# Kernel tuning notes

Measured on AMD Instinct MI355X. Metric: run time of the kernel, lower is better.

The kernel has to match this reference:

```python
import jax, jax.numpy as jnp
import numpy as np

B, DIM, H, W = 16, 96, 64, 64
HID = 2 * DIM          # ffn_expansion_factor = 2
BN_EPS = 1e-5
LN_EPS = 1e-6


def _gelu(x):
    return jax.nn.gelu(x, approximate=False)  # torch F.gelu default = exact erf


def _ln(x, g, b):
    m = jnp.mean(x, axis=-1, keepdims=True)
    v = jnp.mean((x - m) ** 2, axis=-1, keepdims=True)
    return (x - m) / jnp.sqrt(v + LN_EPS) * g + b


def _dwconv2d(x, w, b):
    # x: (B,C,H,W), w: (C,1,kh,kw) depthwise
    C = x.shape[1]
    kh, kw = w.shape[2], w.shape[3]
    y = jax.lax.conv_general_dilated(
        x, w, (1, 1), [(kh // 2, kh // 2), (kw // 2, kw // 2)],
        dimension_numbers=('NCHW', 'OIHW', 'NCHW'), feature_group_count=C)
    return y + b[None, :, None, None]


def _conv_along_c(z, w, b):
    # z: (N,1,C); w: (8,1,k) -> conv over spectral/channel axis (Conv3d with (1,1,k) kernel)
    k = w.shape[2]
    y = jax.lax.conv_general_dilated(z, w, (1,), [(k // 2, k // 2)],
                                     dimension_numbers=('NCH', 'OIH', 'NCH'))
    return y + b[None, :, None]


def _bn_branch(y, g, bb):
    # eval-mode BatchNorm3d with running_mean=0, running_var=1; y: (N,8,C)
    return _gelu(y * (g / jnp.sqrt(1.0 + BN_EPS))[None, :, None] + bb[None, :, None])


def _patch_embed(z, w3a, b3a, bn3a_g, bn3a_b, w3b, b3b, bn3b_g, bn3b_b,
                 w3c, b3c, bn3c_g, bn3c_b, w2, b2, bn2_g, bn2_b):
    # z: (b,h,w,c) NHWC; PatchEmbedLayerSpa
    b_, h_, w_, c_ = z.shape
    zf = z.reshape(-1, 1, c_)
    f1 = _bn_branch(_conv_along_c(zf, w3a, b3a), bn3a_g, bn3a_b)
    f2 = _bn_branch(_conv_along_c(zf, w3b, b3b), bn3b_g, bn3b_b)
    f3 = _bn_branch(_conv_along_c(zf, w3c, b3c), bn3c_g, bn3c_b)
    cat = jnp.concatenate([f1, f2, f3], axis=1).reshape(b_, h_, w_, 24, c_)
    # 1x1 Conv2d over flattened (c y) -> dim; einsum replaces rearrange + conv
    y = jnp.einsum('bhwoy,doy->bhwd', cat, w2) + b2
    y = _gelu(y * (bn2_g / jnp.sqrt(1.0 + BN_EPS)) + bn2_b)  # eval BatchNorm2d + GELU
    return y + z


def _ffn(t, pin_w, pin_b, dw_w, dw_b, pout_w, pout_b):
    # Restormer GDFN; t: (b, c, X, Y) NCHW
    u = jnp.einsum('bcxy,oc->boxy', t, pin_w) + pin_b[None, :, None, None]
    u = _dwconv2d(u, dw_w, dw_b)
    u1, u2 = jnp.split(u, 2, axis=1)
    g = _gelu(u1) * u2
    return jnp.einsum('bcxy,oc->boxy', g, pout_w) + pout_b[None, :, None, None]


def setup_inputs() -> dict:
    key = jax.random.key(0)
    ks = iter(jax.random.split(key, 48))
    nrm = lambda shape, s=0.02: jax.random.normal(next(ks), shape, jnp.float32) * s
    d = {}
    d['x'] = jax.random.normal(next(ks), (B, DIM, H, W), jnp.float32)
    d['pos_w'] = nrm((DIM, 1, 3, 3)); d['pos_b'] = jnp.zeros((DIM,), jnp.float32)
    for n in ('ln1', 'ln2', 'ln3'):
        d[n + '_g'] = jnp.ones((DIM,), jnp.float32)
        d[n + '_b'] = jnp.zeros((DIM,), jnp.float32)
    for n, k in (('a', 3), ('b', 5), ('c', 7)):
        d['w3' + n] = nrm((8, 1, k)); d['b3' + n] = jnp.zeros((8,), jnp.float32)
        d['bn3' + n + '_g'] = jnp.ones((8,), jnp.float32)
        d['bn3' + n + '_b'] = jnp.zeros((8,), jnp.float32)
    d['w2'] = nrm((DIM, 24, DIM)); d['b2'] = jnp.zeros((DIM,), jnp.float32)
    d['bn2_g'] = jnp.ones((DIM,), jnp.float32); d['bn2_b'] = jnp.zeros((DIM,), jnp.float32)
    d['pin_w'] = nrm((2 * HID, DIM)); d['pin_b'] = jnp.zeros((2 * HID,), jnp.float32)
    d['dw_w'] = nrm((2 * HID, 1, 3, 3)); d['dw_b'] = jnp.zeros((2 * HID,), jnp.float32)
    d['pout_w'] = nrm((DIM, HID)); d['pout_b'] = jnp.zeros((DIM,), jnp.float32)
    return d


def reference(x, pos_w, pos_b, ln1_g, ln1_b, ln2_g, ln2_b, ln3_g, ln3_b,
              w3a, b3a, bn3a_g, bn3a_b, w3b, b3b, bn3b_g, bn3b_b,
              w3c, b3c, bn3c_g, bn3c_b, w2, b2, bn2_g, bn2_b,
              pin_w, pin_b, dw_w, dw_b, pout_w, pout_b):
    # pos embed dwconv + residual (NCHW)
    x = x + _dwconv2d(x, pos_w, pos_b)
    y = jnp.transpose(x, (0, 2, 3, 1))  # NHWC
    # attn4(norm3(y)) returns its input (bug in source: `out = rearrange(x, ...)`)
    y = y + _ln(y, ln3_g, ln3_b)
    # attn(norm1(y)) returns PatchEmbedLayerSpa(norm1(y)) (same bug in MGEFE)
    y = y + _patch_embed(_ln(y, ln1_g, ln1_b), w3a, b3a, bn3a_g, bn3a_b,
                         w3b, b3b, bn3b_g, bn3b_b, w3c, b3c, bn3c_g, bn3c_b,
                         w2, b2, bn2_g, bn2_b)
    y = _ln(y, ln2_g, ln2_b)
    t = jnp.transpose(y, (0, 3, 2, 1))  # (b,c,w,h) per source permute(0,3,2,1)
    f = _ffn(t, pin_w, pin_b, dw_w, dw_b, pout_w, pout_b)
    f = jnp.transpose(f, (0, 2, 3, 1))  # (b,w,h,c)
    y = f + f
    return jnp.transpose(y, (0, 3, 1, 2))  # (b,c,w,h)
```

## Files before the change

kernel.cpp:

```cpp
#include <hip/hip_runtime.h>


using bf16x8 = __attribute__((ext_vector_type(8))) short;
using f32x4  = __attribute__((ext_vector_type(4))) float;
using f32x2  = __attribute__((ext_vector_type(2))) float;

struct P {
  const float *x, *pos_w, *pos_b;
  const float *ln1g, *ln1b, *ln2g, *ln2b, *ln3g, *ln3b;
  const float *w3a, *b3a, *bn3ag, *bn3ab;
  const float *w3b, *b3b, *bn3bg, *bn3bb;
  const float *w3c, *b3c, *bn3cg, *bn3cb;
  const float *w2, *b2, *bn2g, *bn2b;
  const float *pin_w, *pin_b, *dw_w, *dw_b, *pout_w, *pout_b;
  unsigned short *u;
  unsigned short *w2f;
  unsigned short *pinf;
  unsigned short *poutf;
  float *dwt;
  float *out;
};

__device__ __forceinline__ unsigned short f2bf(float f) {
  unsigned int v = __float_as_uint(f);
  v += 0x7fffu + ((v >> 16) & 1u);
  return (unsigned short)(v >> 16);
}
__device__ __forceinline__ float bf2f(unsigned short s) {
  return __uint_as_float(((unsigned int)s) << 16);
}
__device__ __forceinline__ unsigned int cvtpk(f32x2 g) {
  unsigned int pk;
  asm("v_cvt_pk_bf16_f32 %0, %1, %2" : "=v"(pk) : "v"(g.x), "v"(g.y));
  return pk;
}

__device__ __forceinline__ f32x2 gelu2p(f32x2 x) {
  f32x2 u = x * 0.70710678118654752f;
  f32x2 s = __builtin_elementwise_min(u * u, f32x2{1.f, 1.f});
  f32x2 pq = __builtin_elementwise_fma(s, f32x2{1.1283585149e-1f, 1.1283585149e-1f},
                                       f32x2{-3.7612625824e-1f, -3.7612625824e-1f});
  pq = __builtin_elementwise_fma(pq, s, f32x2{1.1283791657f, 1.1283791657f});
  f32x2 xh = x * 0.5f;
  return __builtin_elementwise_fma(xh, u * pq, xh);
}

__device__ __forceinline__ void swz_decode(int bid, int& b, int& s) {
  int xcd = bid & 7, idx = bid >> 3;
  b = xcd * 2 + (idx >> 6);
  s = idx & 63;
}

__global__ __launch_bounds__(256) void prep(P p) {
  int id = blockIdx.x * 256 + threadIdx.x;
  if (id < 221184) {
    int j = id & 7, l = (id >> 3) & 63, r = id >> 9;
    int ks = r % 3; r /= 3; int nt = r % 6, o = r / 6;
    int d = nt * 16 + (l & 15), y = ks * 32 + (l >> 4) * 8 + j;
    p.w2f[id] = f2bf(p.w2[(d * 24 + o) * 96 + y]);
  } else if (id < 258048) {
    int id2 = id - 221184;
    int j = id2 & 7, l = (id2 >> 3) & 63, r = id2 >> 9;
    int ks = r % 3, nt = r / 3;
    int o = nt * 16 + (l & 15), k = ks * 32 + (l >> 4) * 8 + j;
    p.pinf[id2] = f2bf(p.pin_w[o * 96 + k]);
  } else if (id < 276480) {
    int id3 = id - 258048;
    int j = id3 & 7, l = (id3 >> 3) & 63, r = id3 >> 9;
    int ks = r % 6, mt = r / 6;
    int d = mt * 16 + (l & 15), cc = ks * 32 + (l >> 4) * 8 + j;
    p.poutf[id3] = f2bf(p.pout_w[d * 192 + cc]);
  } else if (id < 279936) {
    int id4 = id - 276480;
    int tap = id4 / 384, c = id4 - tap * 384;
    p.dwt[id4] = p.dw_w[c * 9 + tap];
  }
}

template <int KSZ>
__device__ __forceinline__ void k2_cat(const float* __restrict__ w3, float b3v,
    float bng, float bnb, float rs, unsigned short* buf,
    const float (&zw)[30], int px, int c0) {
  float sc = bng * rs;
  float wr[KSZ];
  #pragma unroll
  for (int k = 0; k < KSZ; ++k) wr[k] = w3[k] * sc;
  float bias0 = fmaf(b3v, sc, bnb);
  constexpr int OFF = 3 - KSZ / 2;
  unsigned int packed[12];
  #pragma unroll
  for (int e2 = 0; e2 < 12; ++e2) {
    f32x2 f = {bias0, bias0};
    #pragma unroll
    for (int k = 0; k < KSZ; ++k) {
      f32x2 zp = {zw[2 * e2 + OFF + k], zw[2 * e2 + 1 + OFF + k]};
      f = __builtin_elementwise_fma(f32x2{wr[k], wr[k]}, zp, f);
    }
    packed[e2] = cvtpk(gelu2p(f));
  }
  uint4* cw = (uint4*)(buf + px * 104 + c0);
  cw[0] = *(uint4*)&packed[0];
  cw[1] = *(uint4*)&packed[4];
  cw[2] = *(uint4*)&packed[8];
}

template <int KSZ_NEXT, bool LAST>
__device__ __forceinline__ void k2_step(
    const P& p, int o, const float* __restrict__ w3n, float b3n,
    float bngn, float bnbn, float rs,
    const unsigned short* cur, unsigned short* nxt, const float (&zw)[30],
    int px, int c0, int nt0, int ar0, int ar1, f32x4 (&acc)[2][3]) {
  int lane = (threadIdx.x & 63);
  const unsigned short* wf = p.w2f + (size_t)o * 9216 + lane * 8;
  bf16x8 Ba[3], Bb[3];
  #pragma unroll
  for (int n = 0; n < 3; ++n)
    Ba[n] = *(const bf16x8*)(wf + ((nt0 + n) * 3 + 0) * 512);

  if (!LAST)
    k2_cat<KSZ_NEXT>(w3n, b3n, bngn, bnbn, rs, nxt, zw, px, c0);

  #pragma unroll
  for (int n = 0; n < 3; ++n)
    Bb[n] = *(const bf16x8*)(wf + ((nt0 + n) * 3 + 1) * 512);
  {
    bf16x8 a0 = *(const bf16x8*)&cur[ar0];
    bf16x8 a1 = *(const bf16x8*)&cur[ar1];
    #pragma unroll
    for (int n = 0; n < 3; ++n) {
      acc[0][n] = __builtin_amdgcn_mfma_f32_16x16x32_bf16(a0, Ba[n], acc[0][n], 0, 0, 0);
      acc[1][n] = __builtin_amdgcn_mfma_f32_16x16x32_bf16(a1, Ba[n], acc[1][n], 0, 0, 0);
    }
  }
  #pragma unroll
  for (int n = 0; n < 3; ++n)
    Ba[n] = *(const bf16x8*)(wf + ((nt0 + n) * 3 + 2) * 512);
  {
    bf16x8 a0 = *(const bf16x8*)&cur[ar0 + 32];
    bf16x8 a1 = *(const bf16x8*)&cur[ar1 + 32];
    #pragma unroll
    for (int n = 0; n < 3; ++n) {
      acc[0][n] = __builtin_amdgcn_mfma_f32_16x16x32_bf16(a0, Bb[n], acc[0][n], 0, 0, 0);
      acc[1][n] = __builtin_amdgcn_mfma_f32_16x16x32_bf16(a1, Bb[n], acc[1][n], 0, 0, 0);
    }
  }
  {
    bf16x8 a0 = *(const bf16x8*)&cur[ar0 + 64];
    bf16x8 a1 = *(const bf16x8*)&cur[ar1 + 64];
    #pragma unroll
    for (int n = 0; n < 3; ++n) {
      acc[0][n] = __builtin_amdgcn_mfma_f32_16x16x32_bf16(a0, Ba[n], acc[0][n], 0, 0, 0);
      acc[1][n] = __builtin_amdgcn_mfma_f32_16x16x32_bf16(a1, Ba[n], acc[1][n], 0, 0, 0);
    }
  }
  __syncthreads();
}

__global__ __launch_bounds__(256) void k2(P p) {
  __shared__ __align__(16) char smraw[26624];
  unsigned short* cat0 = (unsigned short*)smraw;
  unsigned short* cat1 = (unsigned short*)(smraw + 13312);
  float*          t1   = (float*)smraw;

  int b, h; swz_decode(blockIdx.x, b, h);
  int t = threadIdx.x, lane = t & 63, wv = t >> 6;
  int px = t >> 2, sub = t & 3, c0 = sub * 24;
  const float* xb = p.x + (size_t)b * 96 * 4096;

  if (t < 192) {
    int c = t >> 1, w0 = (t & 1) * 32;
    const float* xc = xb + (size_t)c * 4096;
    float win[3][34];
    #pragma unroll
    for (int r = 0; r < 3; ++r) {
      int hh = h - 1 + r;
      bool v = (hh >= 0 && hh < 64);
      const float* row = xc + hh * 64;
      #pragma unroll
      for (int i = 0; i < 8; ++i) {
        float4 q = v ? *(const float4*)(row + w0 + i * 4) : make_float4(0,0,0,0);
        win[r][1+i*4] = q.x; win[r][2+i*4] = q.y;
        win[r][3+i*4] = q.z; win[r][4+i*4] = q.w;
      }
      win[r][0]  = (v && w0 > 0)  ? row[w0 - 1]  : 0.f;
      win[r][33] = (v && w0 < 32) ? row[w0 + 32] : 0.f;
    }
    float wt[9];
    #pragma unroll
    for (int i = 0; i < 9; ++i) wt[i] = p.pos_w[c * 9 + i];
    float pb = p.pos_b[c];
    #pragma unroll
    for (int w = 0; w < 32; ++w) {
      float acc = pb;
      #pragma unroll
      for (int r = 0; r < 3; ++r)
        #pragma unroll
        for (int j = 0; j < 3; ++j)
          acc = fmaf(wt[r * 3 + j], win[r][w + j], acc);
      t1[c * 65 + w0 + w] = win[1][w + 1] + acc;
    }
  }
  __syncthreads();

  float vv[24];
  float zw[30];
  {
    float s1 = 0.f, s2 = 0.f;
    #pragma unroll
    for (int i = 0; i < 24; ++i) {
      float q = t1[(c0 + i) * 65 + px];
      vv[i] = q; s1 += q; s2 += q * q;
    }
    s1 += __shfl_xor(s1, 1); s1 += __shfl_xor(s1, 2);
    s2 += __shfl_xor(s2, 1); s2 += __shfl_xor(s2, 2);
    float m = s1 * (1.f / 96.f);
    float r = rsqrtf(fmaf(-m, m, s2 * (1.f / 96.f)) + 1e-6f);
    float t1s = 0.f, t2s = 0.f;
    #pragma unroll
    for (int i = 0; i < 24; ++i) {
      int c = c0 + i;
      float y = vv[i] + fmaf((vv[i] - m) * r, p.ln3g[c], p.ln3b[c]);
      vv[i] = y; t1s += y; t2s += y * y;
    }
    t1s += __shfl_xor(t1s, 1); t1s += __shfl_xor(t1s, 2);
    t2s += __shfl_xor(t2s, 1); t2s += __shfl_xor(t2s, 2);
    float m1 = t1s * (1.f / 96.f);
    float r1 = rsqrtf(fmaf(-m1, m1, t2s * (1.f / 96.f)) + 1e-6f);
    #pragma unroll
    for (int i = 0; i < 24; ++i) {
      int c = c0 + i;
      zw[3 + i] = fmaf((vv[i] - m1) * r1, p.ln1g[c], p.ln1b[c]);
    }
  }
  {
    float a0 = __shfl(zw[24], lane - 1), a1 = __shfl(zw[25], lane - 1),
          a2 = __shfl(zw[26], lane - 1);
    float b0 = __shfl(zw[3], lane + 1), b1 = __shfl(zw[4], lane + 1),
          b2 = __shfl(zw[5], lane + 1);
    bool lo = (sub > 0), hi = (sub < 3);
    zw[0] = lo ? a0 : 0.f; zw[1] = lo ? a1 : 0.f; zw[2] = lo ? a2 : 0.f;
    zw[27] = hi ? b0 : 0.f; zw[28] = hi ? b1 : 0.f; zw[29] = hi ? b2 : 0.f;
  }
  __syncthreads();

  const float rs = rsqrtf(1.f + 1e-5f);
  const int m0 = (wv >> 1) * 32, nt0 = (wv & 1) * 3;
  const int lm = lane & 15, lq = lane >> 4;
  const int ar0 = (m0 + lm) * 104 + lq * 8, ar1 = ar0 + 16 * 104;
  f32x4 acc[2][3];
  #pragma unroll
  for (int m = 0; m < 2; ++m)
    #pragma unroll
    for (int n = 0; n < 3; ++n) acc[m][n] = (f32x4){0.f, 0.f, 0.f, 0.f};

  k2_cat<3>(p.w3a, p.b3a[0], p.bn3ag[0], p.bn3ab[0], rs, cat0, zw, px, c0);
  __syncthreads();

  for (int o = 0; o < 7; ++o)
    k2_step<3, false>(p, o, p.w3a + (o + 1) * 3, p.b3a[o + 1],
                      p.bn3ag[o + 1], p.bn3ab[o + 1], rs,
                      (o & 1) ? cat1 : cat0, (o & 1) ? cat0 : cat1,
                      zw, px, c0, nt0, ar0, ar1, acc);
  k2_step<5, false>(p, 7, p.w3b, p.b3b[0], p.bn3bg[0], p.bn3bb[0], rs,
                    cat1, cat0, zw, px, c0, nt0, ar0, ar1, acc);
  for (int o = 8; o < 15; ++o)
    k2_step<5, false>(p, o, p.w3b + (o - 7) * 5, p.b3b[o - 7],
                      p.bn3bg[o - 7], p.bn3bb[o - 7], rs,
                      (o & 1) ? cat1 : cat0, (o & 1) ? cat0 : cat1,
                      zw, px, c0, nt0, ar0, ar1, acc);
  k2_step<7, false>(p, 15, p.w3c, p.b3c[0], p.bn3cg[0], p.bn3cb[0], rs,
                    cat1, cat0, zw, px, c0, nt0, ar0, ar1, acc);
  for (int o = 16; o < 23; ++o)
    k2_step<7, false>(p, o, p.w3c + (o - 15) * 7, p.b3c[o - 15],
                      p.bn3cg[o - 15], p.bn3cb[o - 15], rs,
                      (o & 1) ? cat1 : cat0, (o & 1) ? cat0 : cat1,
                      zw, px, c0, nt0, ar0, ar1, acc);
  k2_step<3, true>(p, 23, p.w3a, 0.f, 0.f, 0.f, rs,
                   cat1, cat0, zw, px, c0, nt0, ar0, ar1, acc);

  #pragma unroll
  for (int mi = 0; mi < 2; ++mi)
    #pragma unroll
    for (int n = 0; n < 3; ++n) {
      int d = (nt0 + n) * 16 + lm;
      float sc2 = p.bn2g[d] * rs, sh2 = p.bn2b[d], bias = p.b2[d];
      int pxb = m0 + mi * 16 + lq * 4;
      unsigned int pk01 = cvtpk(gelu2p(f32x2{fmaf(acc[mi][n][0] + bias, sc2, sh2),
                                             fmaf(acc[mi][n][1] + bias, sc2, sh2)}));
      unsigned int pk23 = cvtpk(gelu2p(f32x2{fmaf(acc[mi][n][2] + bias, sc2, sh2),
                                             fmaf(acc[mi][n][3] + bias, sc2, sh2)}));
      cat0[(pxb+0) * 104 + d] = (unsigned short)(pk01 & 0xffffu);
      cat0[(pxb+1) * 104 + d] = (unsigned short)(pk01 >> 16);
      cat0[(pxb+2) * 104 + d] = (unsigned short)(pk23 & 0xffffu);
      cat0[(pxb+3) * 104 + d] = (unsigned short)(pk23 >> 16);
    }
  __syncthreads();

  {
    const unsigned int* gsrc = (const unsigned int*)(cat0 + px * 104 + c0);
    float s1 = 0.f, s2 = 0.f;
    #pragma unroll
    for (int i2 = 0; i2 < 6; ++i2) {
      unsigned int w0 = gsrc[i2 * 2], w1 = gsrc[i2 * 2 + 1];
      float g0 = __uint_as_float(w0 << 16), g1 = __uint_as_float(w0 & 0xffff0000u);
      float g2 = __uint_as_float(w1 << 16), g3 = __uint_as_float(w1 & 0xffff0000u);
      float y0v = g0 + zw[3 + i2*4 + 0] + vv[i2*4 + 0];
      float y1v = g1 + zw[3 + i2*4 + 1] + vv[i2*4 + 1];
      float y2v = g2 + zw[3 + i2*4 + 2] + vv[i2*4 + 2];
      float y3v = g3 + zw[3 + i2*4 + 3] + vv[i2*4 + 3];
      vv[i2*4+0] = y0v; vv[i2*4+1] = y1v; vv[i2*4+2] = y2v; vv[i2*4+3] = y3v;
      s1 += y0v + y1v + y2v + y3v;
      s2 += y0v*y0v + y1v*y1v + y2v*y2v + y3v*y3v;
    }
    s1 += __shfl_xor(s1, 1); s1 += __shfl_xor(s1, 2);
    s2 += __shfl_xor(s2, 1); s2 += __shfl_xor(s2, 2);
    float m = s1 * (1.f / 96.f);
    float r = rsqrtf(fmaf(-m, m, s2 * (1.f / 96.f)) + 1e-6f);
    unsigned int* dst = (unsigned int*)(cat1 + px * 104 + c0);
    #pragma unroll
    for (int i = 0; i < 12; ++i) {
      int c = c0 + 2 * i;
      f32x2 y3p = {fmaf((vv[2*i]   - m) * r, p.ln2g[c],     p.ln2b[c]),
                   fmaf((vv[2*i+1] - m) * r, p.ln2g[c + 1], p.ln2b[c + 1])};
      dst[i] = cvtpk(y3p);
    }
  }
  __syncthreads();

  {
    const int mt = wv;
    bf16x8 B3[3];
    #pragma unroll
    for (int ks = 0; ks < 3; ++ks)
      B3[ks] = *(const bf16x8*)&cat1[(mt * 16 + lm) * 104 + ks * 32 + lq * 8];
    unsigned short* ubh = p.u + (size_t)b * 1572864 + h * 384;
    const int w = mt * 16 + lm;
    unsigned short* urow = ubh + (size_t)w * 24576 + lq * 4;

    bf16x8 An[3];
    const unsigned short* pf0 = p.pinf + lane * 8;
    #pragma unroll
    for (int ks = 0; ks < 3; ++ks)
      An[ks] = *(const bf16x8*)(pf0 + ks * 512);
    for (int nt = 0; nt < 24; ++nt) {
      bf16x8 Af[3] = {An[0], An[1], An[2]};
      if (nt < 23) {
        const unsigned short* pf = p.pinf + ((nt + 1) * 3) * 512 + lane * 8;
        #pragma unroll
        for (int ks = 0; ks < 3; ++ks)
          An[ks] = *(const bf16x8*)(pf + ks * 512);
      }
      f32x4 a4 = (f32x4){0.f, 0.f, 0.f, 0.f};
      #pragma unroll
      for (int ks = 0; ks < 3; ++ks)
        a4 = __builtin_amdgcn_mfma_f32_16x16x32_bf16(Af[ks], B3[ks], a4, 0, 0, 0);
      float4 pbq = *(const float4*)(p.pin_b + nt * 16 + lq * 4);
      unsigned int lo = cvtpk(f32x2{a4[0] + pbq.x, a4[1] + pbq.y});
      unsigned int hi = cvtpk(f32x2{a4[2] + pbq.z, a4[3] + pbq.w});
      *(uint2*)(urow + nt * 16) = make_uint2(lo, hi);
    }
  }
}

__global__ __launch_bounds__(192) void k4(P p) {
  __shared__ __align__(16) char sm4[40960];
  float*          dwl = (float*)sm4;
  float*          dbl = (float*)(sm4 + 13824);
  unsigned short* gl  = (unsigned short*)(sm4 + 15360);

  int b, w; swz_decode(blockIdx.x, b, w);
  int t = threadIdx.x, lane = t & 63, wv = t >> 6;
  const unsigned short* ub = p.u + (size_t)b * 1572864;

  for (int id = t; id < 3456; id += 192) dwl[id] = p.dwt[id];
  for (int id = t; id < 384; id += 192) dbl[id] = p.dw_b[id];
  __syncthreads();

  {
    int g = t / 24, cb = t - g * 24;
    int c0 = cb * 8, hb = g * 8;
    float4 b1a = *(const float4*)&dbl[c0],       b1b = *(const float4*)&dbl[c0 + 4];
    float4 b2a = *(const float4*)&dbl[192 + c0], b2b = *(const float4*)&dbl[196 + c0];
    const bf16x8 zv = {0,0,0,0,0,0,0,0};
    for (int kk = 0; kk < 4; ++kk) {
      int h0 = hb + kk * 2;
      float v1[2][8], v2[2][8];
      #pragma unroll
      for (int hr = 0; hr < 2; ++hr) {
        v1[hr][0]=b1a.x; v1[hr][1]=b1a.y; v1[hr][2]=b1a.z; v1[hr][3]=b1a.w;
        v1[hr][4]=b1b.x; v1[hr][5]=b1b.y; v1[hr][6]=b1b.z; v1[hr][7]=b1b.w;
        v2[hr][0]=b2a.x; v2[hr][1]=b2a.y; v2[hr][2]=b2a.z; v2[hr][3]=b2a.w;
        v2[hr][4]=b2b.x; v2[hr][5]=b2b.y; v2[hr][6]=b2b.z; v2[hr][7]=b2b.w;
      }
      #pragma unroll
      for (int dw_ = -1; dw_ <= 1; ++dw_) {
        int ww = w + dw_;
        if (ww < 0 || ww > 63) continue;
        bf16x8 r1[4], r2[4];
        #pragma unroll
        for (int rr = 0; rr < 4; ++rr) {
          int hh = h0 - 1 + rr;
          bool ok = (hh >= 0 && hh <= 63);
          const unsigned short* up = ub + ((size_t)ww * 64 + hh) * 384 + c0;
          r1[rr] = ok ? *(const bf16x8*)up : zv;
          r2[rr] = ok ? *(const bf16x8*)(up + 192) : zv;
        }
        #pragma unroll
        for (int dh = -1; dh <= 1; ++dh) {
          int tap = (dw_ + 1) * 3 + (dh + 1);
          float4 w1a = *(const float4*)&dwl[tap * 384 + c0];
          float4 w1b = *(const float4*)&dwl[tap * 384 + c0 + 4];
          float4 w2a = *(const float4*)&dwl[tap * 384 + 192 + c0];
          float4 w2b = *(const float4*)&dwl[tap * 384 + 196 + c0];
          float wt1[8] = {w1a.x,w1a.y,w1a.z,w1a.w,w1b.x,w1b.y,w1b.z,w1b.w};
          float wt2[8] = {w2a.x,w2a.y,w2a.z,w2a.w,w2b.x,w2b.y,w2b.z,w2b.w};
          #pragma unroll
          for (int hr = 0; hr < 2; ++hr) {
            int rr = hr + dh + 1;
            #pragma unroll
            for (int j = 0; j < 8; ++j) {
              v1[hr][j] = fmaf(wt1[j], bf2f((unsigned short)r1[rr][j]), v1[hr][j]);
              v2[hr][j] = fmaf(wt2[j], bf2f((unsigned short)r2[rr][j]), v2[hr][j]);
            }
          }
        }
      }
      #pragma unroll
      for (int hr = 0; hr < 2; ++hr) {
        unsigned int pk4[4];
        #pragma unroll
        for (int j2 = 0; j2 < 4; ++j2) {
          f32x2 a = {v1[hr][2*j2], v1[hr][2*j2+1]};
          f32x2 bv = {v2[hr][2*j2], v2[hr][2*j2+1]};
          pk4[j2] = cvtpk(gelu2p(a) * bv);
        }
        uint2* dst = (uint2*)(gl + (h0 + hr) * 200 + c0);
        dst[0] = make_uint2(pk4[0], pk4[1]);
        dst[1] = make_uint2(pk4[2], pk4[3]);
      }
    }
  }
  __syncthreads();

  const int lm = lane & 15, lq = lane >> 4;
  const int mtb = wv * 2;
  bf16x8 Af[2][6];
  const unsigned short* pof = p.poutf + lane * 8;
  #pragma unroll
  for (int mi = 0; mi < 2; ++mi)
    #pragma unroll
    for (int ks = 0; ks < 6; ++ks)
      Af[mi][ks] = *(const bf16x8*)(pof + ((mtb + mi) * 6 + ks) * 512);
  f32x4 acc[2][4];
  #pragma unroll
  for (int mi = 0; mi < 2; ++mi)
    #pragma unroll
    for (int n = 0; n < 4; ++n) acc[mi][n] = (f32x4){0.f, 0.f, 0.f, 0.f};
  #pragma unroll
  for (int ks = 0; ks < 6; ++ks) {
    bf16x8 Bg[4];
    #pragma unroll
    for (int n = 0; n < 4; ++n)
      Bg[n] = *(const bf16x8*)&gl[(n * 16 + lm) * 200 + ks * 32 + lq * 8];
    #pragma unroll
    for (int mi = 0; mi < 2; ++mi)
      #pragma unroll
      for (int n = 0; n < 4; ++n)
        acc[mi][n] = __builtin_amdgcn_mfma_f32_16x16x32_bf16(Af[mi][ks], Bg[n], acc[mi][n], 0, 0, 0);
  }
  float* ob = p.out + (size_t)b * 393216 + (size_t)w * 64;
  #pragma unroll
  for (int mi = 0; mi < 2; ++mi)
    #pragma unroll
    for (int r = 0; r < 4; ++r) {
      int d = (mtb + mi) * 16 + lq * 4 + r;
      float pb = p.pout_b[d];
      #pragma unroll
      for (int n = 0; n < 4; ++n) {
        int hcol = n * 16 + lm;
        ob[(size_t)d * 4096 + hcol] = 2.f * (acc[mi][n][r] + pb);
      }
    }
}

extern "C" void kernel_launch(void* const* d_in, const int* in_sizes, int n_in,
                              void* d_out, int out_size, void* d_ws, size_t ws_size,
                              hipStream_t stream) {
  (void)in_sizes; (void)n_in; (void)out_size; (void)ws_size;
  P p;
  p.x     = (const float*)d_in[0];
  p.pos_w = (const float*)d_in[1];  p.pos_b = (const float*)d_in[2];
  p.ln1g  = (const float*)d_in[3];  p.ln1b  = (const float*)d_in[4];
  p.ln2g  = (const float*)d_in[5];  p.ln2b  = (const float*)d_in[6];
  p.ln3g  = (const float*)d_in[7];  p.ln3b  = (const float*)d_in[8];
  p.w3a   = (const float*)d_in[9];  p.b3a   = (const float*)d_in[10];
  p.bn3ag = (const float*)d_in[11]; p.bn3ab = (const float*)d_in[12];
  p.w3b   = (const float*)d_in[13]; p.b3b   = (const float*)d_in[14];
  p.bn3bg = (const float*)d_in[15]; p.bn3bb = (const float*)d_in[16];
  p.w3c   = (const float*)d_in[17]; p.b3c   = (const float*)d_in[18];
  p.bn3cg = (const float*)d_in[19]; p.bn3cb = (const float*)d_in[20];
  p.w2    = (const float*)d_in[21]; p.b2    = (const float*)d_in[22];
  p.bn2g  = (const float*)d_in[23]; p.bn2b  = (const float*)d_in[24];
  p.pin_w = (const float*)d_in[25]; p.pin_b = (const float*)d_in[26];
  p.dw_w  = (const float*)d_in[27]; p.dw_b  = (const float*)d_in[28];
  p.pout_w= (const float*)d_in[29]; p.pout_b= (const float*)d_in[30];

  char* ws = (char*)d_ws;
  p.u     = (unsigned short*)ws;
  p.poutf = (unsigned short*)(ws + 50331648);
  p.dwt   = (float*)(ws + 50368512);
  p.w2f   = (unsigned short*)d_out;
  p.pinf  = (unsigned short*)((char*)d_out + 442368);
  p.out   = (float*)d_out;

  prep<<<dim3(1094), dim3(256), 0, stream>>>(p);
  k2 <<<dim3(1024), dim3(256), 0, stream>>>(p);
  k4 <<<dim3(1024), dim3(192), 0, stream>>>(p);
}
```

Baseline: 151.0 us.

## Process two cat slices per barrier using a quad-buffered LDS pipeline

Changes the patch-embed conv/GEMM loop so each barrier interval covers two cat slices. Four LDS buffers replace two, so two slices are produced while the previous pair is consumed by MFMA. This halves the number of __syncthreads in the 24-step loop. In exchange it doubles the LDS footprint to 52 KB per block, which may lower occupancy, and increases unrolled code size.

```diff
diff --git a/kernel.cpp b/kernel.cpp
--- a/kernel.cpp
+++ b/kernel.cpp
@@ -104,22 +104,14 @@
   cw[2] = *(uint4*)&packed[8];
 }
 
-template <int KSZ_NEXT, bool LAST>
-__device__ __forceinline__ void k2_step(
-    const P& p, int o, const float* __restrict__ w3n, float b3n,
-    float bngn, float bnbn, float rs,
-    const unsigned short* cur, unsigned short* nxt, const float (&zw)[30],
-    int px, int c0, int nt0, int ar0, int ar1, f32x4 (&acc)[2][3]) {
+__device__ __forceinline__ void k2_mfma(const P& p, int o,
+    const unsigned short* cur, int nt0, int ar0, int ar1, f32x4 (&acc)[2][3]) {
   int lane = (threadIdx.x & 63);
   const unsigned short* wf = p.w2f + (size_t)o * 9216 + lane * 8;
   bf16x8 Ba[3], Bb[3];
   #pragma unroll
   for (int n = 0; n < 3; ++n)
     Ba[n] = *(const bf16x8*)(wf + ((nt0 + n) * 3 + 0) * 512);
-
-  if (!LAST)
-    k2_cat<KSZ_NEXT>(w3n, b3n, bngn, bnbn, rs, nxt, zw, px, c0);
-
   #pragma unroll
   for (int n = 0; n < 3; ++n)
     Bb[n] = *(const bf16x8*)(wf + ((nt0 + n) * 3 + 1) * 512);
@@ -153,14 +145,14 @@
       acc[1][n] = __builtin_amdgcn_mfma_f32_16x16x32_bf16(a1, Ba[n], acc[1][n], 0, 0, 0);
     }
   }
-  __syncthreads();
 }
 
 __global__ __launch_bounds__(256) void k2(P p) {
-  __shared__ __align__(16) char smraw[26624];
-  unsigned short* cat0 = (unsigned short*)smraw;
-  unsigned short* cat1 = (unsigned short*)(smraw + 13312);
-  float*          t1   = (float*)smraw;
+  __shared__ __align__(16) char smraw[53248];
+  unsigned short* cbuf[4] = {
+    (unsigned short*)smraw,            (unsigned short*)(smraw + 13312),
+    (unsigned short*)(smraw + 26624),  (unsigned short*)(smraw + 39936)};
+  float* t1 = (float*)smraw;
 
   int b, h; swz_decode(blockIdx.x, b, h);
   int t = threadIdx.x, lane = t & 63, wv = t >> 6;
@@ -253,31 +245,61 @@
     #pragma unroll
     for (int n = 0; n < 3; ++n) acc[m][n] = (f32x4){0.f, 0.f, 0.f, 0.f};
 
-  k2_cat<3>(p.w3a, p.b3a[0], p.bn3ag[0], p.bn3ab[0], rs, cat0, zw, px, c0);
-  __syncthreads();
-
-  for (int o = 0; o < 7; ++o)
-    k2_step<3, false>(p, o, p.w3a + (o + 1) * 3, p.b3a[o + 1],
-                      p.bn3ag[o + 1], p.bn3ab[o + 1], rs,
-                      (o & 1) ? cat1 : cat0, (o & 1) ? cat0 : cat1,
-                      zw, px, c0, nt0, ar0, ar1, acc);
-  k2_step<5, false>(p, 7, p.w3b, p.b3b[0], p.bn3bg[0], p.bn3bb[0], rs,
-                    cat1, cat0, zw, px, c0, nt0, ar0, ar1, acc);
-  for (int o = 8; o < 15; ++o)
-    k2_step<5, false>(p, o, p.w3b + (o - 7) * 5, p.b3b[o - 7],
-                      p.bn3bg[o - 7], p.bn3bb[o - 7], rs,
-                      (o & 1) ? cat1 : cat0, (o & 1) ? cat0 : cat1,
-                      zw, px, c0, nt0, ar0, ar1, acc);
-  k2_step<7, false>(p, 15, p.w3c, p.b3c[0], p.bn3cg[0], p.bn3cb[0], rs,
-                    cat1, cat0, zw, px, c0, nt0, ar0, ar1, acc);
-  for (int o = 16; o < 23; ++o)
-    k2_step<7, false>(p, o, p.w3c + (o - 15) * 7, p.b3c[o - 15],
-                      p.bn3cg[o - 15], p.bn3cb[o - 15], rs,
-                      (o & 1) ? cat1 : cat0, (o & 1) ? cat0 : cat1,
-                      zw, px, c0, nt0, ar0, ar1, acc);
-  k2_step<3, true>(p, 23, p.w3a, 0.f, 0.f, 0.f, rs,
-                   cat1, cat0, zw, px, c0, nt0, ar0, ar1, acc);
-
+  k2_cat<3>(p.w3a,     p.b3a[0], p.bn3ag[0], p.bn3ab[0], rs, cbuf[0], zw, px, c0);
+  k2_cat<3>(p.w3a + 3, p.b3a[1], p.bn3ag[1], p.bn3ab[1], rs, cbuf[1], zw, px, c0);
+  __syncthreads();
+
+  #pragma unroll
+  for (int i = 0; i < 3; ++i) {
+    int o = 2 * i;
+    const unsigned short* rA = cbuf[(i & 1) ? 2 : 0];
+    const unsigned short* rB = cbuf[(i & 1) ? 3 : 1];
+    unsigned short* wA = cbuf[(i & 1) ? 0 : 2];
+    unsigned short* wB = cbuf[(i & 1) ? 1 : 3];
+    k2_mfma(p, o, rA, nt0, ar0, ar1, acc);
+    k2_cat<3>(p.w3a + (o + 2) * 3, p.b3a[o + 2], p.bn3ag[o + 2], p.bn3ab[o + 2],
+              rs, wA, zw, px, c0);
+    k2_mfma(p, o + 1, rB, nt0, ar0, ar1, acc);
+    k2_cat<3>(p.w3a + (o + 3) * 3, p.b3a[o + 3], p.bn3ag[o + 3], p.bn3ab[o + 3],
+              rs, wB, zw, px, c0);
+    __syncthreads();
+  }
+  #pragma unroll
+  for (int i = 3; i < 7; ++i) {
+    int o = 2 * i;
+    const unsigned short* rA = cbuf[(i & 1) ? 2 : 0];
+    const unsigned short* rB = cbuf[(i & 1) ? 3 : 1];
+    unsigned short* wA = cbuf[(i & 1) ? 0 : 2];
+    unsigned short* wB = cbuf[(i & 1) ? 1 : 3];
+    int ca = o + 2 - 8, cb2 = o + 3 - 8;
+    k2_mfma(p, o, rA, nt0, ar0, ar1, acc);
+    k2_cat<5>(p.w3b + ca * 5, p.b3b[ca], p.bn3bg[ca], p.bn3bb[ca],
+              rs, wA, zw, px, c0);
+    k2_mfma(p, o + 1, rB, nt0, ar0, ar1, acc);
+    k2_cat<5>(p.w3b + cb2 * 5, p.b3b[cb2], p.bn3bg[cb2], p.bn3bb[cb2],
+              rs, wB, zw, px, c0);
+    __syncthreads();
+  }
+  #pragma unroll
+  for (int i = 7; i < 11; ++i) {
+    int o = 2 * i;
+    const unsigned short* rA = cbuf[(i & 1) ? 2 : 0];
+    const unsigned short* rB = cbuf[(i & 1) ? 3 : 1];
+    unsigned short* wA = cbuf[(i & 1) ? 0 : 2];
+    unsigned short* wB = cbuf[(i & 1) ? 1 : 3];
+    int ca = o + 2 - 16, cb2 = o + 3 - 16;
+    k2_mfma(p, o, rA, nt0, ar0, ar1, acc);
+    k2_cat<7>(p.w3c + ca * 7, p.b3c[ca], p.bn3cg[ca], p.bn3cb[ca],
+              rs, wA, zw, px, c0);
+    k2_mfma(p, o + 1, rB, nt0, ar0, ar1, acc);
+    k2_cat<7>(p.w3c + cb2 * 7, p.b3c[cb2], p.bn3cg[cb2], p.bn3cb[cb2],
+              rs, wB, zw, px, c0);
+    __syncthreads();
+  }
+  k2_mfma(p, 22, cbuf[2], nt0, ar0, ar1, acc);
+  k2_mfma(p, 23, cbuf[3], nt0, ar0, ar1, acc);
+
+  unsigned short* g0 = cbuf[0];
   #pragma unroll
   for (int mi = 0; mi < 2; ++mi)
     #pragma unroll
@@ -289,25 +311,26 @@
                                              fmaf(acc[mi][n][1] + bias, sc2, sh2)}));
       unsigned int pk23 = cvtpk(gelu2p(f32x2{fmaf(acc[mi][n][2] + bias, sc2, sh2),
                                              fmaf(acc[mi][n][3] + bias, sc2, sh2)}));
-      cat0[(pxb+0) * 104 + d] = (unsigned short)(pk01 & 0xffffu);
-      cat0[(pxb+1) * 104 + d] = (unsigned short)(pk01 >> 16);
-      cat0[(pxb+2) * 104 + d] = (unsigned short)(pk23 & 0xffffu);
-      cat0[(pxb+3) * 104 + d] = (unsigned short)(pk23 >> 16);
-    }
-  __syncthreads();
-
-  {
-    const unsigned int* gsrc = (const unsigned int*)(cat0 + px * 104 + c0);
+      g0[(pxb+0) * 104 + d] = (unsigned short)(pk01 & 0xffffu);
+      g0[(pxb+1) * 104 + d] = (unsigned short)(pk01 >> 16);
+      g0[(pxb+2) * 104 + d] = (unsigned short)(pk23 & 0xffffu);
+      g0[(pxb+3) * 104 + d] = (unsigned short)(pk23 >> 16);
+    }
+  __syncthreads();
+
+  unsigned short* y3b = cbuf[1];
+  {
+    const unsigned int* gsrc = (const unsigned int*)(g0 + px * 104 + c0);
     float s1 = 0.f, s2 = 0.f;
     #pragma unroll
     for (int i2 = 0; i2 < 6; ++i2) {
       unsigned int w0 = gsrc[i2 * 2], w1 = gsrc[i2 * 2 + 1];
-      float g0 = __uint_as_float(w0 << 16), g1 = __uint_as_float(w0 & 0xffff0000u);
-      float g2 = __uint_as_float(w1 << 16), g3 = __uint_as_float(w1 & 0xffff0000u);
-      float y0v = g0 + zw[3 + i2*4 + 0] + vv[i2*4 + 0];
-      float y1v = g1 + zw[3 + i2*4 + 1] + vv[i2*4 + 1];
-      float y2v = g2 + zw[3 + i2*4 + 2] + vv[i2*4 + 2];
-      float y3v = g3 + zw[3 + i2*4 + 3] + vv[i2*4 + 3];
+      float g0v = __uint_as_float(w0 << 16), g1v = __uint_as_float(w0 & 0xffff0000u);
+      float g2v = __uint_as_float(w1 << 16), g3v = __uint_as_float(w1 & 0xffff0000u);
+      float y0v = g0v + zw[3 + i2*4 + 0] + vv[i2*4 + 0];
+      float y1v = g1v + zw[3 + i2*4 + 1] + vv[i2*4 + 1];
+      float y2v = g2v + zw[3 + i2*4 + 2] + vv[i2*4 + 2];
+      float y3v = g3v + zw[3 + i2*4 + 3] + vv[i2*4 + 3];
       vv[i2*4+0] = y0v; vv[i2*4+1] = y1v; vv[i2*4+2] = y2v; vv[i2*4+3] = y3v;
       s1 += y0v + y1v + y2v + y3v;
       s2 += y0v*y0v + y1v*y1v + y2v*y2v + y3v*y3v;
@@ -316,7 +339,7 @@
     s2 += __shfl_xor(s2, 1); s2 += __shfl_xor(s2, 2);
     float m = s1 * (1.f / 96.f);
     float r = rsqrtf(fmaf(-m, m, s2 * (1.f / 96.f)) + 1e-6f);
-    unsigned int* dst = (unsigned int*)(cat1 + px * 104 + c0);
+    unsigned int* dst = (unsigned int*)(y3b + px * 104 + c0);
     #pragma unroll
     for (int i = 0; i < 12; ++i) {
       int c = c0 + 2 * i;
@@ -332,7 +355,7 @@
     bf16x8 B3[3];
     #pragma unroll
     for (int ks = 0; ks < 3; ++ks)
-      B3[ks] = *(const bf16x8*)&cat1[(mt * 16 + lm) * 104 + ks * 32 + lq * 8];
+      B3[ks] = *(const bf16x8*)&y3b[(mt * 16 + lm) * 104 + ks * 32 + lq * 8];
     unsigned short* ubh = p.u + (size_t)b * 1572864 + h * 384;
     const int w = mt * 16 + lm;
     unsigned short* urow = ubh + (size_t)w * 24576 + lq * 4;
```

Result: slower. 166.0 us (+9.9%).
